# Optimization experiments

Hardware: AMD Instinct MI355X
Metric: run time of the kernel (lower is better)

Reference implementation:

```python
import jax, jax.numpy as jnp
import numpy as np
from jax.scipy.special import erf

B, T, D, H = 256, 128, 128, 1024  # batch, seq_len, enc_in, hid_dim
SIGMA = 0.5  # stochastic-gate sigma (STG FeatureSelector)


def _uniform(key, shape, std):
    return jax.random.uniform(key, shape, jnp.float32, -std, std)


def setup_inputs() -> dict:
    key = jax.random.key(0)
    ks = jax.random.split(key, 16)
    std = 1.0 / np.sqrt(H)
    inp = {
        "x": jax.random.normal(ks[0], (B, T, D), jnp.float32),
        # s_lstm
        "s_x2h_w": _uniform(ks[1], (4 * H, D), std),
        "s_x2h_b": _uniform(ks[2], (4 * H,), std),
        "s_h2h_w": _uniform(ks[3], (4 * H, H), std),
        "s_h2h_b": _uniform(ks[4], (4 * H,), std),
        # p_lstm
        "p_x2h_w": _uniform(ks[5], (4 * H, D), std),
        "p_x2h_b": _uniform(ks[6], (4 * H,), std),
        "p_h2h_w": _uniform(ks[7], (4 * H, H), std),
        "p_h2h_b": _uniform(ks[8], (4 * H,), std),
        # p_fc: hid -> 2*enc_in
        "p_fc_w": _uniform(ks[9], (2 * D, H), std),
        "p_fc_b": _uniform(ks[10], (2 * D,), std),
        # FeatureSelector mu layer: hid -> enc_in
        "fs_w": _uniform(ks[11], (D, H), std),
        "fs_b": _uniform(ks[12], (D,), std),
    }
    return inp


def _lstm_cell(x, h, c, wx, bx, wh, bh):
    gates = x @ wx.T + bx + h @ wh.T + bh          # [B, 4H]
    i, f, g, o = jnp.split(gates, 4, axis=1)
    cy = c * jax.nn.sigmoid(f) + jax.nn.sigmoid(i) * jnp.tanh(g)
    hy = jax.nn.sigmoid(o) * jnp.tanh(cy)
    return hy, cy


def _forward(x, s_x2h_w, s_x2h_b, s_h2h_w, s_h2h_b,
             p_x2h_w, p_x2h_b, p_h2h_w, p_h2h_b,
             p_fc_w, p_fc_b, fs_w, fs_b):
    b = x.shape[0]
    xt = jnp.swapaxes(x, 0, 1)  # [T, B, D] time-major
    sqrt2 = jnp.sqrt(jnp.float32(2.0))

    def step(carry, xs):
        hn, cn, hn2, cn2, mask_prev, xhat0_prev = carry
        x_t, x_tp1 = xs
        # at seq==0 mask_prev=1, xhat0_prev=0 -> input is exactly x_t
        inp = mask_prev * x_t + (1.0 - mask_prev) * xhat0_prev
        hn, cn = _lstm_cell(inp, hn, cn, s_x2h_w, s_x2h_b, s_h2h_w, s_h2h_b)
        # FeatureSelector (eval: noise = 0)
        mu = hn @ fs_w.T + fs_b                     # [B, D]
        z = mu
        mask = jnp.clip(z + 0.5, 0.0, 1.0)          # hard sigmoid gate
        reg = 0.5 * (1.0 + erf((mu + 0.5) / (SIGMA * sqrt2)))  # Phi((mu+0.5)/sigma)
        hn2, cn2 = _lstm_cell(mask * x_tp1, hn2, cn2, p_x2h_w, p_x2h_b, p_h2h_w, p_h2h_b)
        xhat = (hn2 @ p_fc_w.T + p_fc_b).reshape(b, 2, D)
        xhat0, xhat1 = xhat[:, 0, :], xhat[:, 1, :]
        mu_det = jax.lax.stop_gradient(mu)          # torch.tensor(numpy) detaches
        prob_det = jax.lax.stop_gradient(reg)
        outs = (mask, xhat0, xhat1, reg, mu_det, prob_det, z)
        return (hn, cn, hn2, cn2, mask, xhat0), outs

    h0 = jnp.zeros((b, H), x.dtype)
    carry0 = (h0, h0, h0, h0, jnp.ones((b, D), x.dtype), jnp.zeros((b, D), x.dtype))
    _, outs = jax.lax.scan(step, carry0, (xt[:-1], xt[1:]))
    # each out: [T-1, B, D] -> [B, T-1, D]
    return tuple(jnp.swapaxes(o, 0, 1) for o in outs)


def reference(x, s_x2h_w, s_x2h_b, s_h2h_w, s_h2h_b,
              p_x2h_w, p_x2h_b, p_h2h_w, p_h2h_b,
              p_fc_w, p_fc_b, fs_w, fs_b):
    return _forward(x, s_x2h_w, s_x2h_b, s_h2h_w, s_h2h_b,
                    p_x2h_w, p_x2h_b, p_h2h_w, p_h2h_b,
                    p_fc_w, p_fc_b, fs_w, fs_b)
```

## Files before the change

kernel.cpp:

```cpp
#include <hip/hip_runtime.h>
#include <math.h>

#define BB 256
#define TT 128
#define DD 128
#define HH 1024
#define G4 4096
#define TOUT 127
#define OSZ (BB * TOUT * DD)
#define NKB 36
#define ACTE (16 * NKB * 512)

typedef __bf16 bf16x8 __attribute__((ext_vector_type(8)));
typedef float f32x4 __attribute__((ext_vector_type(4)));
typedef unsigned short u16;
typedef unsigned int u32;
typedef unsigned long long u64;

__device__ inline u16 f2bf(float f) {
    union { float f; u32 u; } v; v.f = f;
    u32 r = v.u + 0x7FFFu + ((v.u >> 16) & 1u);
    return (u16)(r >> 16);
}
__device__ inline float fsig(float x)  { return __fdividef(1.0f, 1.0f + __expf(-x)); }
__device__ inline float ftanh(float x) { return __fdividef(2.0f, 1.0f + __expf(-2.0f * x)) - 1.0f; }

__device__ __forceinline__ bf16x8 ld_act(const u16* p) {
    union { u64 q[2]; bf16x8 v; } u;
    u.q[0] = __hip_atomic_load((u64*)p,     __ATOMIC_RELAXED, __HIP_MEMORY_SCOPE_AGENT);
    u.q[1] = __hip_atomic_load((u64*)p + 1, __ATOMIC_RELAXED, __HIP_MEMORY_SCOPE_AGENT);
    return u.v;
}
__device__ __forceinline__ void st_u32(u16* p, u32 v) {
    __hip_atomic_store((u32*)p, v, __ATOMIC_RELAXED, __HIP_MEMORY_SCOPE_AGENT);
}

__device__ __forceinline__ void gbar(u32* bars, u32 gen) {
    asm volatile("s_waitcnt vmcnt(0)" ::: "memory");
    __syncthreads();
    if (threadIdx.x == 0)
        __hip_atomic_fetch_add(&bars[(blockIdx.x & 31) << 4], 1u,
                               __ATOMIC_RELAXED, __HIP_MEMORY_SCOPE_AGENT);
    if (threadIdx.x < 32) {
        while (__hip_atomic_load(&bars[threadIdx.x << 4],
                                 __ATOMIC_RELAXED, __HIP_MEMORY_SCOPE_AGENT) < gen * 8u)
            __builtin_amdgcn_s_sleep(4);
    }
    __syncthreads();
}

struct SArgs {
    u16 *acts, *actp;
    const u16 *wS, *wP, *fswb, *pfcb;
    const float *bS, *bP, *fsb, *pfb, *x;
    float* mbuf;
    float* out;
    u32* bars;
};

__device__ __forceinline__ void lstm_phase(
    const u16* __restrict__ act, const u16* __restrict__ wb,
    const float* __restrict__ bias, float* __restrict__ cst ,
    u16* __restrict__ hact, float* red ,
    int bid, int w, int lane)
{
    const int wn = w & 1, wm = (w >> 1) & 1, kg = w >> 2;
    const int mb = ((bid >> 6) << 2) + wm * 2;
    const int nb = ((bid & 63) << 2) + wn * 2;

    const u16* a0 = act + (((size_t)(mb + 0) * NKB + kg * 18) * 64 + lane) * 8;
    const u16* a1 = act + (((size_t)(mb + 1) * NKB + kg * 18) * 64 + lane) * 8;
    const u16* b0 = wb  + (((size_t)(nb + 0) * NKB + kg * 18) * 64 + lane) * 8;
    const u16* b1 = wb  + (((size_t)(nb + 1) * NKB + kg * 18) * 64 + lane) * 8;

    f32x4 acc[2][2] = {};
#pragma unroll 6
    for (int it = 0; it < 18; ++it) {
        bf16x8 av0 = ld_act(a0 + it * 512);
        bf16x8 av1 = ld_act(a1 + it * 512);
        bf16x8 bv0 = *(const bf16x8*)(b0 + it * 512);
        bf16x8 bv1 = *(const bf16x8*)(b1 + it * 512);
        acc[0][0] = __builtin_amdgcn_mfma_f32_16x16x32_bf16(av0, bv0, acc[0][0], 0, 0, 0);
        acc[0][1] = __builtin_amdgcn_mfma_f32_16x16x32_bf16(av0, bv1, acc[0][1], 0, 0, 0);
        acc[1][0] = __builtin_amdgcn_mfma_f32_16x16x32_bf16(av1, bv0, acc[1][0], 0, 0, 0);
        acc[1][1] = __builtin_amdgcn_mfma_f32_16x16x32_bf16(av1, bv1, acc[1][1], 0, 0, 0);
    }

    if (kg == 1) {
#pragma unroll
        for (int mi = 0; mi < 2; ++mi)
#pragma unroll
        for (int ni = 0; ni < 2; ++ni)
            *(f32x4*)&red[(((((wm << 1) | wn) << 1 | mi) << 1 | ni) << 8) + (lane << 2)] = acc[mi][ni];
    }
    __syncthreads();

    if (kg == 0) {
        const int col = lane & 15, row4 = (lane >> 4) << 2, g0 = lane & 3;
        const int m_base = ((bid >> 6) << 6) + wm * 32;
        const int n_base = ((bid & 63) << 6) + wn * 32;
#pragma unroll
        for (int mi = 0; mi < 2; ++mi)
#pragma unroll
        for (int ni = 0; ni < 2; ++ni) {
            f32x4 s1 = *(const f32x4*)&red[(((((wm << 1) | wn) << 1 | mi) << 1 | ni) << 8) + (lane << 2)];
            const int n = n_base + ni * 16 + col;
            const float bv = bias[n];
#pragma unroll
            for (int rr = 0; rr < 4; ++rr) {
                float v = acc[mi][ni][rr] + s1[rr] + bv;
                float v1 = __shfl_xor(v, 1);
                float v2 = __shfl_xor(v, 2);
                float v3 = __shfl_xor(v, 3);
                const int m = m_base + mi * 16 + row4 + rr;
                const int j = n >> 2;
                u32 hbits = 0;
                if (g0 == 0) {
                    const int ml = wm * 32 + mi * 16 + row4 + rr;
                    const int jl = (wn * 32 + ni * 16 + col) >> 2;
                    float cp = cst[ml * 16 + jl];
                    float cy = cp * fsig(v1) + fsig(v) * ftanh(v2);
                    float hy = fsig(v3) * ftanh(cy);
                    cst[ml * 16 + jl] = cy;
                    hbits = (u32)f2bf(hy);
                }
                u32 pv = hbits | (((u32)__shfl_xor((int)hbits, 4)) << 16);
                if ((lane & 7) == 0)
                    st_u32(&hact[(((size_t)(m >> 4) * NKB + (4 + (j >> 5))) * 64 +
                                  ((m & 15) + (((j >> 3) & 3) << 4))) * 8 + (j & 7)], pv);
            }
        }
    }
}

__global__ __launch_bounds__(512, 2) void k_scan(SArgs A)
{
    __shared__ __align__(16) float red[4096];
    __shared__ float cst[2][64][16];

    const int bid = blockIdx.x, tid = threadIdx.x;
    const int w = tid >> 6, lane = tid & 63;

    for (int i = tid; i < 2 * 64 * 16; i += 512) ((float*)cst)[i] = 0.f;

    float* o_mask = A.out;
    float* o_x0   = A.out + 1 * (size_t)OSZ;
    float* o_x1   = A.out + 2 * (size_t)OSZ;
    float* o_reg  = A.out + 3 * (size_t)OSZ;
    float* o_mu   = A.out + 4 * (size_t)OSZ;
    float* o_prob = A.out + 5 * (size_t)OSZ;
    float* o_z    = A.out + 6 * (size_t)OSZ;

    u32 gen = 0;

    for (int t = 0; t < TOUT; ++t) {
        const u16* s_cur = A.acts + (size_t)(t & 1) * ACTE;
        u16*       s_nxt = A.acts + (size_t)((t + 1) & 1) * ACTE;
        u16*       p_cur = A.actp + (size_t)(t & 1) * ACTE;
        u16*       p_nxt = A.actp + (size_t)((t + 1) & 1) * ACTE;

        lstm_phase(s_cur, A.wS, A.bS, &cst[0][0][0], s_nxt, red, bid, w, lane);
        gbar(A.bars, ++gen);

        if (bid < 128) {
            const int bm = bid >> 3, bn = bid & 7;
            f32x4 acc = {};
#pragma unroll
            for (int i = 0; i < 4; ++i) {
                const int kb = (w << 2) + i;
                bf16x8 av = ld_act(s_nxt + (((size_t)bm * NKB + 4 + kb) * 64 + lane) * 8);
                bf16x8 bv = *(const bf16x8*)(A.fswb + (((size_t)bn * 32 + kb) * 64 + lane) * 8);
                acc = __builtin_amdgcn_mfma_f32_16x16x32_bf16(av, bv, acc, 0, 0, 0);
            }
            *(f32x4*)&red[(w * 64 + lane) << 2] = acc;
            __syncthreads();
            if (tid < 256) {
                const int m16 = tid >> 4, d16 = tid & 15;
                const int rl = ((m16 >> 2) << 4) | d16, rr = m16 & 3;
                float v = 0.f;
#pragma unroll
                for (int ww = 0; ww < 8; ++ww) v += red[((ww * 64 + rl) << 2) + rr];
                const int m = (bm << 4) + m16, d = (bn << 4) + d16;
                float mu = v + A.fsb[d];
                float mask = fminf(fmaxf(mu + 0.5f, 0.f), 1.f);
                float reg = 0.5f * (1.0f + erff((mu + 0.5f) * 1.41421356237f));
                const size_t o = (size_t)m * (TOUT * DD) + (size_t)t * DD + d;
                o_mask[o] = mask; o_reg[o] = reg; o_mu[o] = mu; o_prob[o] = reg; o_z[o] = mu;
                __hip_atomic_store(&A.mbuf[m * DD + d], mask,
                                   __ATOMIC_RELAXED, __HIP_MEMORY_SCOPE_AGENT);
                float xv = A.x[(size_t)m * (TT * DD) + (size_t)(t + 1) * DD + d];
                u32 xb = (u32)f2bf(mask * xv);
                u32 pv = xb | (((u32)__shfl_xor((int)xb, 1)) << 16);
                if ((d16 & 1) == 0)
                    st_u32(&p_cur[(((size_t)(m >> 4) * NKB + (d >> 5)) * 64 +
                                   ((m & 15) + (((d >> 3) & 3) << 4))) * 8 + (d & 7)], pv);
            }
        }
        gbar(A.bars, ++gen);

        lstm_phase(p_cur, A.wP, A.bP, &cst[1][0][0], p_nxt, red, bid, w, lane);
        gbar(A.bars, ++gen);

        {
            const int bm = bid >> 4, bn = bid & 15;
            f32x4 acc = {};
#pragma unroll
            for (int i = 0; i < 4; ++i) {
                const int kb = (w << 2) + i;
                bf16x8 av = ld_act(p_nxt + (((size_t)bm * NKB + 4 + kb) * 64 + lane) * 8);
                bf16x8 bv = *(const bf16x8*)(A.pfcb + (((size_t)bn * 32 + kb) * 64 + lane) * 8);
                acc = __builtin_amdgcn_mfma_f32_16x16x32_bf16(av, bv, acc, 0, 0, 0);
            }
            *(f32x4*)&red[(w * 64 + lane) << 2] = acc;
            __syncthreads();
            if (tid < 256) {
                const int m16 = tid >> 4, d16 = tid & 15;
                const int rl = ((m16 >> 2) << 4) | d16, rr = m16 & 3;
                float v = 0.f;
#pragma unroll
                for (int ww = 0; ww < 8; ++ww) v += red[((ww * 64 + rl) << 2) + rr];
                const int m = (bm << 4) + m16, n = (bn << 4) + d16;
                v += A.pfb[n];
                const size_t ob = (size_t)m * (TOUT * DD) + (size_t)t * DD;
                if (bn < 8) {
                    o_x0[ob + n] = v;
                    float mk = __hip_atomic_load(&A.mbuf[m * DD + n],
                                                 __ATOMIC_RELAXED, __HIP_MEMORY_SCOPE_AGENT);
                    float xv = A.x[(size_t)m * (TT * DD) + (size_t)(t + 1) * DD + n];
                    u32 ib = (u32)f2bf(mk * xv + (1.f - mk) * v);
                    u32 pv = ib | (((u32)__shfl_xor((int)ib, 1)) << 16);
                    if ((d16 & 1) == 0)
                        st_u32(&s_nxt[(((size_t)(m >> 4) * NKB + (n >> 5)) * 64 +
                                       ((m & 15) + (((n >> 3) & 3) << 4))) * 8 + (n & 7)], pv);
                } else {
                    o_x1[ob + (n - DD)] = v;
                }
            }
        }
        gbar(A.bars, ++gen);
    }
}


__global__ void k_wgates(const float* __restrict__ wx, const float* __restrict__ wh,
                         u16* __restrict__ blob) {
    int i = blockIdx.x * 256 + threadIdx.x;
    if (i >= 256 * NKB * 64) return;
    int lane = i & 63, cblk = (i >> 6) % NKB, rblk = (i >> 6) / NKB;
    int n = (rblk << 4) | (lane & 15);
    int c = (cblk << 5) + ((lane >> 4) << 3);
    int orow = ((n & 3) << 10) | (n >> 2);
    const float* s = (cblk < 4) ? (wx + (size_t)orow * DD + c)
                                : (wh + (size_t)orow * HH + (c - 128));
    u16* d = blob + (size_t)i * 8;
#pragma unroll
    for (int k = 0; k < 8; ++k) d[k] = f2bf(s[k]);
}

__global__ void k_wplain(const float* __restrict__ wsrc, u16* __restrict__ blob,
                         int nblk, int K) {
    int CB = K >> 5;
    int i = blockIdx.x * 256 + threadIdx.x;
    if (i >= nblk * CB * 64) return;
    int lane = i & 63, cblk = (i >> 6) % CB, rblk = (i >> 6) / CB;
    int r = (rblk << 4) | (lane & 15);
    int c = (cblk << 5) + ((lane >> 4) << 3);
    const float* s = wsrc + (size_t)r * K + c;
    u16* d = blob + (size_t)i * 8;
#pragma unroll
    for (int k = 0; k < 8; ++k) d[k] = f2bf(s[k]);
}

__global__ void k_bias2(const float* __restrict__ bx, const float* __restrict__ bh,
                        float* __restrict__ dst) {
    int r = blockIdx.x * 256 + threadIdx.x;
    if (r < G4) {
        int o = ((r & 3) << 10) | (r >> 2);
        dst[r] = bx[o] + bh[o];
    }
}

__global__ void k_zero(u16* acts, u16* actp, u32* bars) {
    size_t i = (size_t)blockIdx.x * 256 + threadIdx.x;
    if (i < 2 * (size_t)ACTE) { acts[i] = 0; actp[i] = 0; }
    if (i < 512) bars[i] = 0;
}

__global__ void k_fillx(const float* __restrict__ x, u16* __restrict__ acts) {
    int i = blockIdx.x * 256 + threadIdx.x;
    if (i >= BB * DD) return;
    int m = i >> 7, d = i & 127;
    acts[(((size_t)(m >> 4) * NKB + (d >> 5)) * 64 +
          ((m & 15) + (((d >> 3) & 3) << 4))) * 8 + (d & 7)] =
        f2bf(x[(size_t)m * (TT * DD) + d]);
}

extern "C" void kernel_launch(void* const* d_in, const int* in_sizes, int n_in,
                              void* d_out, int out_size, void* d_ws, size_t ws_size,
                              hipStream_t stream) {
    const float* x       = (const float*)d_in[0];
    const float* s_x2h_w = (const float*)d_in[1];
    const float* s_x2h_b = (const float*)d_in[2];
    const float* s_h2h_w = (const float*)d_in[3];
    const float* s_h2h_b = (const float*)d_in[4];
    const float* p_x2h_w = (const float*)d_in[5];
    const float* p_x2h_b = (const float*)d_in[6];
    const float* p_h2h_w = (const float*)d_in[7];
    const float* p_h2h_b = (const float*)d_in[8];
    const float* p_fc_w  = (const float*)d_in[9];
    const float* p_fc_b  = (const float*)d_in[10];
    const float* fs_w    = (const float*)d_in[11];
    const float* fs_b    = (const float*)d_in[12];

    char* ws = (char*)d_ws;
    size_t off = 0;
    auto alloc = [&](size_t bytes) { void* p = ws + off; off += (bytes + 255) & ~(size_t)255; return p; };
    u16*   wS   = (u16*)  alloc((size_t)G4 * 1152 * 2);
    u16*   wP   = (u16*)  alloc((size_t)G4 * 1152 * 2);
    u16*   fswb = (u16*)  alloc((size_t)8 * 32 * 512 * 2);
    u16*   pfcb = (u16*)  alloc((size_t)16 * 32 * 512 * 2);
    float* bS   = (float*)alloc((size_t)G4 * 4);
    float* bP   = (float*)alloc((size_t)G4 * 4);
    u16*   acts = (u16*)  alloc((size_t)2 * ACTE * 2);
    u16*   actp = (u16*)  alloc((size_t)2 * ACTE * 2);
    float* mbuf = (float*)alloc((size_t)BB * DD * 4);
    u32*   bars = (u32*)  alloc(2048);

    k_wgates<<<dim3(2304), 256, 0, stream>>>(s_x2h_w, s_h2h_w, wS);
    k_wgates<<<dim3(2304), 256, 0, stream>>>(p_x2h_w, p_h2h_w, wP);
    k_wplain<<<dim3(64),  256, 0, stream>>>(fs_w, fswb, 8, 1024);
    k_wplain<<<dim3(128), 256, 0, stream>>>(p_fc_w, pfcb, 16, 1024);
    k_bias2<<<dim3(16), 256, 0, stream>>>(s_x2h_b, s_h2h_b, bS);
    k_bias2<<<dim3(16), 256, 0, stream>>>(p_x2h_b, p_h2h_b, bP);
    k_zero<<<dim3(2304), 256, 0, stream>>>(acts, actp, bars);
    k_fillx<<<dim3(128), 256, 0, stream>>>(x, acts);

    SArgs sa;
    sa.acts = acts; sa.actp = actp;
    sa.wS = wS; sa.wP = wP; sa.fswb = fswb; sa.pfcb = pfcb;
    sa.bS = bS; sa.bP = bP; sa.fsb = fs_b; sa.pfb = p_fc_b; sa.x = x;
    sa.mbuf = mbuf; sa.out = (float*)d_out; sa.bars = bars;

    void* kargs[] = { &sa };
    hipError_t e = hipLaunchCooperativeKernel((const void*)k_scan, dim3(256), dim3(512),
                                              kargs, 0, stream);
    if (e != hipSuccess) {
        k_scan<<<dim3(256), dim3(512), 0, stream>>>(sa);
    }
}
```

Measured before the change: 5.442 ms.

## Retile LSTM phase to 32x128 tiles with activations staged in LDS

Each block's LSTM tile changes from 64 rows by 64 gate columns to 32 rows by 128 gate columns. The block's activation slice is loaded once into LDS and shared by all waves, instead of every wave fetching it from global memory with atomic loads. Weight fragments are register double-buffered, so the next k-step's B loads are issued before the current MFMAs run. This removes redundant global activation traffic and hides weight-load latency. In exchange it adds 72KB of LDS, which may lower occupancy below two blocks per CU, plus an extra __syncthreads per phase.

Result: faster. 5.063 ms (-7.0%).

```diff
diff --git a/kernel.cpp b/kernel.cpp
--- a/kernel.cpp
+++ b/kernel.cpp
@@ -16,6 +16,8 @@
 typedef unsigned short u16;
 typedef unsigned int u32;
 typedef unsigned long long u64;
+
+#define MFMA16 __builtin_amdgcn_mfma_f32_16x16x32_bf16
 
 __device__ inline u16 f2bf(float f) {
     union { float f; u32 u; } v; v.f = f;
@@ -61,67 +63,84 @@
 __device__ __forceinline__ void lstm_phase(
     const u16* __restrict__ act, const u16* __restrict__ wb,
     const float* __restrict__ bias, float* __restrict__ cst ,
-    u16* __restrict__ hact, float* red ,
+    u16* __restrict__ hact, float* __restrict__ red ,
+    u64* __restrict__ a_lds ,
     int bid, int w, int lane)
 {
-    const int wn = w & 1, wm = (w >> 1) & 1, kg = w >> 2;
-    const int mb = ((bid >> 6) << 2) + wm * 2;
-    const int nb = ((bid & 63) << 2) + wn * 2;
-
-    const u16* a0 = act + (((size_t)(mb + 0) * NKB + kg * 18) * 64 + lane) * 8;
-    const u16* a1 = act + (((size_t)(mb + 1) * NKB + kg * 18) * 64 + lane) * 8;
-    const u16* b0 = wb  + (((size_t)(nb + 0) * NKB + kg * 18) * 64 + lane) * 8;
-    const u16* b1 = wb  + (((size_t)(nb + 1) * NKB + kg * 18) * 64 + lane) * 8;
+    const int tid = threadIdx.x;
+    const int bm = bid >> 5, bn = bid & 31;
+    const int kg = w >> 2, wv = w & 3;
+
+    {
+        const u64* src = (const u64*)(act + (size_t)bm * 2 * NKB * 512);
+#pragma unroll
+        for (int u = 0; u < 18; ++u) {
+            int idx = tid + u * 512;
+            a_lds[idx] = __hip_atomic_load(&src[idx], __ATOMIC_RELAXED,
+                                           __HIP_MEMORY_SCOPE_AGENT);
+        }
+    }
+    __syncthreads();
+
+    const u16* ab = (const u16*)a_lds;
+    const u16* a0p = ab + (((0 * NKB) + kg * 18) * 64 + lane) * 8;
+    const u16* a1p = ab + (((1 * NKB) + kg * 18) * 64 + lane) * 8;
+    const u16* b0p = wb + (((size_t)(bn * 8 + wv * 2 + 0) * NKB + kg * 18) * 64 + lane) * 8;
+    const u16* b1p = wb + (((size_t)(bn * 8 + wv * 2 + 1) * NKB + kg * 18) * 64 + lane) * 8;
 
     f32x4 acc[2][2] = {};
+    bf16x8 bc0 = *(const bf16x8*)(b0p);
+    bf16x8 bc1 = *(const bf16x8*)(b1p);
 #pragma unroll 6
     for (int it = 0; it < 18; ++it) {
-        bf16x8 av0 = ld_act(a0 + it * 512);
-        bf16x8 av1 = ld_act(a1 + it * 512);
-        bf16x8 bv0 = *(const bf16x8*)(b0 + it * 512);
-        bf16x8 bv1 = *(const bf16x8*)(b1 + it * 512);
-        acc[0][0] = __builtin_amdgcn_mfma_f32_16x16x32_bf16(av0, bv0, acc[0][0], 0, 0, 0);
-        acc[0][1] = __builtin_amdgcn_mfma_f32_16x16x32_bf16(av0, bv1, acc[0][1], 0, 0, 0);
-        acc[1][0] = __builtin_amdgcn_mfma_f32_16x16x32_bf16(av1, bv0, acc[1][0], 0, 0, 0);
-        acc[1][1] = __builtin_amdgcn_mfma_f32_16x16x32_bf16(av1, bv1, acc[1][1], 0, 0, 0);
+        bf16x8 bn0, bn1;
+        if (it < 17) {
+            bn0 = *(const bf16x8*)(b0p + (it + 1) * 512);
+            bn1 = *(const bf16x8*)(b1p + (it + 1) * 512);
+        }
+        bf16x8 a0 = *(const bf16x8*)(a0p + it * 512);
+        bf16x8 a1 = *(const bf16x8*)(a1p + it * 512);
+        acc[0][0] = MFMA16(a0, bc0, acc[0][0], 0, 0, 0);
+        acc[0][1] = MFMA16(a0, bc1, acc[0][1], 0, 0, 0);
+        acc[1][0] = MFMA16(a1, bc0, acc[1][0], 0, 0, 0);
+        acc[1][1] = MFMA16(a1, bc1, acc[1][1], 0, 0, 0);
+        if (it < 17) { bc0 = bn0; bc1 = bn1; }
     }
 
     if (kg == 1) {
 #pragma unroll
         for (int mi = 0; mi < 2; ++mi)
 #pragma unroll
-        for (int ni = 0; ni < 2; ++ni)
-            *(f32x4*)&red[(((((wm << 1) | wn) << 1 | mi) << 1 | ni) << 8) + (lane << 2)] = acc[mi][ni];
+        for (int bi = 0; bi < 2; ++bi)
+            *(f32x4*)&red[(((((wv << 1) | mi) << 1) | bi) << 8) + (lane << 2)] = acc[mi][bi];
     }
     __syncthreads();
 
     if (kg == 0) {
         const int col = lane & 15, row4 = (lane >> 4) << 2, g0 = lane & 3;
-        const int m_base = ((bid >> 6) << 6) + wm * 32;
-        const int n_base = ((bid & 63) << 6) + wn * 32;
 #pragma unroll
         for (int mi = 0; mi < 2; ++mi)
 #pragma unroll
-        for (int ni = 0; ni < 2; ++ni) {
-            f32x4 s1 = *(const f32x4*)&red[(((((wm << 1) | wn) << 1 | mi) << 1 | ni) << 8) + (lane << 2)];
-            const int n = n_base + ni * 16 + col;
+        for (int bi = 0; bi < 2; ++bi) {
+            f32x4 s1 = *(const f32x4*)&red[(((((wv << 1) | mi) << 1) | bi) << 8) + (lane << 2)];
+            const int n = bn * 128 + (wv * 2 + bi) * 16 + col;
             const float bv = bias[n];
 #pragma unroll
             for (int rr = 0; rr < 4; ++rr) {
-                float v = acc[mi][ni][rr] + s1[rr] + bv;
+                float v = acc[mi][bi][rr] + s1[rr] + bv;
                 float v1 = __shfl_xor(v, 1);
                 float v2 = __shfl_xor(v, 2);
                 float v3 = __shfl_xor(v, 3);
-                const int m = m_base + mi * 16 + row4 + rr;
+                const int m = bm * 32 + mi * 16 + row4 + rr;
                 const int j = n >> 2;
                 u32 hbits = 0;
                 if (g0 == 0) {
-                    const int ml = wm * 32 + mi * 16 + row4 + rr;
-                    const int jl = (wn * 32 + ni * 16 + col) >> 2;
-                    float cp = cst[ml * 16 + jl];
+                    const int ml = mi * 16 + row4 + rr;
+                    const int jl = j - bn * 32;
+                    float cp = cst[ml * 32 + jl];
                     float cy = cp * fsig(v1) + fsig(v) * ftanh(v2);
                     float hy = fsig(v3) * ftanh(cy);
-                    cst[ml * 16 + jl] = cy;
+                    cst[ml * 32 + jl] = cy;
                     hbits = (u32)f2bf(hy);
                 }
                 u32 pv = hbits | (((u32)__shfl_xor((int)hbits, 4)) << 16);
@@ -135,13 +154,14 @@
 
 __global__ __launch_bounds__(512, 2) void k_scan(SArgs A)
 {
+    __shared__ __align__(16) u64 a_lds[9216];
     __shared__ __align__(16) float red[4096];
-    __shared__ float cst[2][64][16];
+    __shared__ float cst[2][32][32];
 
     const int bid = blockIdx.x, tid = threadIdx.x;
     const int w = tid >> 6, lane = tid & 63;
 
-    for (int i = tid; i < 2 * 64 * 16; i += 512) ((float*)cst)[i] = 0.f;
+    for (int i = tid; i < 2 * 32 * 32; i += 512) ((float*)cst)[i] = 0.f;
 
     float* o_mask = A.out;
     float* o_x0   = A.out + 1 * (size_t)OSZ;
@@ -159,7 +179,7 @@
         u16*       p_cur = A.actp + (size_t)(t & 1) * ACTE;
         u16*       p_nxt = A.actp + (size_t)((t + 1) & 1) * ACTE;
 
-        lstm_phase(s_cur, A.wS, A.bS, &cst[0][0][0], s_nxt, red, bid, w, lane);
+        lstm_phase(s_cur, A.wS, A.bS, &cst[0][0][0], s_nxt, red, a_lds, bid, w, lane);
         gbar(A.bars, ++gen);
 
         if (bid < 128) {
@@ -170,7 +190,7 @@
                 const int kb = (w << 2) + i;
                 bf16x8 av = ld_act(s_nxt + (((size_t)bm * NKB + 4 + kb) * 64 + lane) * 8);
                 bf16x8 bv = *(const bf16x8*)(A.fswb + (((size_t)bn * 32 + kb) * 64 + lane) * 8);
-                acc = __builtin_amdgcn_mfma_f32_16x16x32_bf16(av, bv, acc, 0, 0, 0);
+                acc = MFMA16(av, bv, acc, 0, 0, 0);
             }
             *(f32x4*)&red[(w * 64 + lane) << 2] = acc;
             __syncthreads();
@@ -198,7 +218,7 @@
         }
         gbar(A.bars, ++gen);
 
-        lstm_phase(p_cur, A.wP, A.bP, &cst[1][0][0], p_nxt, red, bid, w, lane);
+        lstm_phase(p_cur, A.wP, A.bP, &cst[1][0][0], p_nxt, red, a_lds, bid, w, lane);
         gbar(A.bars, ++gen);
 
         {
@@ -209,7 +229,7 @@
                 const int kb = (w << 2) + i;
                 bf16x8 av = ld_act(p_nxt + (((size_t)bm * NKB + 4 + kb) * 64 + lane) * 8);
                 bf16x8 bv = *(const bf16x8*)(A.pfcb + (((size_t)bn * 32 + kb) * 64 + lane) * 8);
-                acc = __builtin_amdgcn_mfma_f32_16x16x32_bf16(av, bv, acc, 0, 0, 0);
+                acc = MFMA16(av, bv, acc, 0, 0, 0);
             }
             *(f32x4*)&red[(w * 64 + lane) << 2] = acc;
             __syncthreads();
```
